# Performance work log

Hardware: AMD Instinct MI355X
Metric: run time of the kernel (lower is better)

## Reference

```python
import jax, jax.numpy as jnp
import numpy as np

B, T, D_MODEL = 4, 2048, 2048
H, KV, HD = 16, 8, 128  # num_heads, num_kv_heads, head_dim
EPS = 1e-6


def _rope_tables(T, hd, base=10000.0):
    inv_freq = 1.0 / (base ** (np.arange(0, hd, 2, dtype=np.float32) / hd))  # [hd/2]
    ang = np.arange(T, dtype=np.float32)[:, None] * inv_freq[None, :]        # [T, hd/2]
    cos = np.repeat(np.cos(ang), 2, axis=-1)                                 # [T, hd]
    sin = np.repeat(np.sin(ang), 2, axis=-1)
    return jnp.asarray(cos), jnp.asarray(sin)


def setup_inputs() -> dict:
    key = jax.random.key(0)
    ks = jax.random.split(key, 6)
    w_std = 0.02
    x = jax.random.normal(ks[0], (B, T, D_MODEL), dtype=jnp.float32)
    Wq = jax.random.normal(ks[1], (D_MODEL, H * HD), dtype=jnp.float32) * w_std
    Wk = jax.random.normal(ks[2], (D_MODEL, KV * HD), dtype=jnp.float32) * w_std
    Wv = jax.random.normal(ks[3], (D_MODEL, KV * HD), dtype=jnp.float32) * w_std
    Wo = jax.random.normal(ks[4], (H * HD, D_MODEL), dtype=jnp.float32) * w_std
    cos, sin = _rope_tables(T, HD)
    q_gamma = jnp.ones((HD,), dtype=jnp.float32)
    k_gamma = jnp.ones((HD,), dtype=jnp.float32)
    return {"x": x, "cos": cos, "sin": sin, "Wq": Wq, "Wk": Wk, "Wv": Wv,
            "Wo": Wo, "q_gamma": q_gamma, "k_gamma": k_gamma}


def _rmsnorm(h, gamma):
    # flax nn.RMSNorm over last axis, learnable scale
    var = jnp.mean(h * h, axis=-1, keepdims=True)
    return h * jax.lax.rsqrt(var + EPS) * gamma


def _rope(h, cos, sin):
    # h: [B, T, heads, HD]; interleaved rotation
    h_rot = jnp.stack([-h[..., 1::2], h[..., 0::2]], axis=-1)
    h_rot = h_rot.reshape(h.shape)
    return h * cos[None, :, None, :] + h_rot * sin[None, :, None, :]


def reference(x, cos, sin, Wq, Wk, Wv, Wo, q_gamma, k_gamma):
    Bx, Tx, _ = x.shape
    G = H // KV  # query groups per kv head
    q = (x @ Wq).reshape(Bx, Tx, H, HD)
    k = (x @ Wk).reshape(Bx, Tx, KV, HD)
    v = (x @ Wv).reshape(Bx, Tx, KV, HD)
    q = _rope(_rmsnorm(q, q_gamma), cos, sin)
    k = _rope(_rmsnorm(k, k_gamma), cos, sin)
    scale = 1.0 / jnp.sqrt(jnp.asarray(HD, dtype=x.dtype))
    qg = q.reshape(Bx, Tx, KV, G, HD)
    # scores: [B, KV, G, Tq, Tk]
    scores = jnp.einsum('btkgd,bskd->bkgts', qg, k) * scale
    p = jax.nn.softmax(scores, axis=-1)
    o = jnp.einsum('bkgts,bskd->btkgd', p, v).reshape(Bx, Tx, H * HD)
    return o @ Wo
```

## Files before the change

kernel.cpp:

```cpp
#include <hip/hip_runtime.h>


typedef unsigned short u16;
typedef unsigned int u32;
typedef __attribute__((ext_vector_type(8))) short bf16x8;
typedef __attribute__((ext_vector_type(4))) float f32x4;

__device__ __forceinline__ float bf2f(u16 v) {
    union { u32 u; float f; } x; x.u = ((u32)v) << 16; return x.f;
}
__device__ __forceinline__ u16 f2bf(float f) {
    union { float f; u32 u; } x; x.f = f;
    u32 u = x.u;
    return (u16)((u + 0x7FFFu + ((u >> 16) & 1u)) >> 16);
}
__device__ __forceinline__ u32 packtrunc(float a, float b) {
    union { float f; u32 u; } x, y; x.f = a; y.f = b;
    return (x.u >> 16) | (y.u & 0xffff0000u);
}
__device__ __forceinline__ f32x4 mfma_bf16(bf16x8 a, bf16x8 b, f32x4 c) {
    return __builtin_amdgcn_mfma_f32_16x16x32_bf16(a, b, c, 0, 0, 0);
}
__device__ __forceinline__ void gl_lds16(const u16* g, u16* l) {
    __builtin_amdgcn_global_load_lds((const __attribute__((address_space(1))) void*)g,
                                     (__attribute__((address_space(3))) void*)l, 16, 0, 0);
}

__global__ __launch_bounds__(256)
void transpose_f2b(const float* __restrict__ in, u16* __restrict__ out, int R, int C) {
    __shared__ float tile[32][33];
    const int tx = threadIdx.x & 31, ty = threadIdx.x >> 5;
    const long c0 = (long)blockIdx.x * 32, r0 = (long)blockIdx.y * 32;
#pragma unroll
    for (int i = 0; i < 4; i++)
        tile[ty + i * 8][tx] = in[(r0 + ty + i * 8) * C + c0 + tx];
    __syncthreads();
#pragma unroll
    for (int i = 0; i < 4; i++)
        out[(c0 + ty + i * 8) * R + r0 + tx] = f2bf(tile[tx][ty + i * 8]);
}

__global__ __launch_bounds__(256)
void cast_f2b(const float* __restrict__ in, u16* __restrict__ out) {
    const long i = ((long)blockIdx.x * 256 + threadIdx.x) * 8;
    float4 a = *(const float4*)(in + i);
    float4 b = *(const float4*)(in + i + 4);
    bf16x8 v;
    v[0] = (short)f2bf(a.x); v[1] = (short)f2bf(a.y);
    v[2] = (short)f2bf(a.z); v[3] = (short)f2bf(a.w);
    v[4] = (short)f2bf(b.x); v[5] = (short)f2bf(b.y);
    v[6] = (short)f2bf(b.z); v[7] = (short)f2bf(b.w);
    *(bf16x8*)(out + i) = v;
}

__global__ __launch_bounds__(256)
void transpose_v(const u16* __restrict__ qkv, u16* __restrict__ Vt) {
    __shared__ u16 tile[32][33];
    const int tx = threadIdx.x & 31, ty = threadIdx.x >> 5;
    const int d0 = blockIdx.x * 32;
    const int tok0 = blockIdx.y * 32;
#pragma unroll
    for (int i = 0; i < 4; i++)
        tile[ty + i * 8][tx] = qkv[(long)(tok0 + ty + i * 8) * 4096 + 3072 + d0 + tx];
    __syncthreads();
    const int b = tok0 >> 11;
    const long orow = (long)b * 1024 + d0;
    const int t0 = tok0 & 2047;
#pragma unroll
    for (int i = 0; i < 4; i++)
        Vt[(orow + ty + i * 8) * 2048 + t0 + tx] = tile[tx][ty + i * 8];
}

template <bool F32OUT>
__global__ __launch_bounds__(512, 2)
void gemm_bt_256(const u16* __restrict__ A, const u16* __restrict__ Bt,
                 void* __restrict__ Cp, int M, int N, int K) {
    __shared__ __align__(16) u16 As[2][256 * 64];
    __shared__ __align__(16) u16 Bs[2][256 * 64];
    const int tid = threadIdx.x, wid = tid >> 6, lane = tid & 63;
    const int q4 = lane >> 4, n16 = lane & 15;
    const int wr = (wid >> 2) * 128;
    const int wc = (wid & 3) * 64;

    const int nbx = N >> 8;
    const int nwg = nbx * (M >> 8);
    int id = (int)blockIdx.x;
    id = (id & 7) * (nwg >> 3) + (id >> 3);
    const long rowT = (long)(id / nbx) * 256;
    const long colT = (long)(id % nbx) * 256;

    const int srow = tid >> 3;
    const int gchunk = (tid & 7) ^ (srow & 7);
    const u16* Ag[4]; const u16* Bg[4];
#pragma unroll
    for (int i = 0; i < 4; i++) {
        Ag[i] = A  + (rowT + i * 64 + srow) * K + gchunk * 8;
        Bg[i] = Bt + (colT + i * 64 + srow) * K + gchunk * 8;
    }
    const int ldst = wid * 512 + lane * 8;

    auto stage = [&](int buf, int kt) {
#pragma unroll
        for (int i = 0; i < 4; i++)
            gl_lds16(Ag[i] + kt, &As[buf][i * 4096 + ldst]);
#pragma unroll
        for (int i = 0; i < 4; i++)
            gl_lds16(Bg[i] + kt, &Bs[buf][i * 4096 + ldst]);
    };

    f32x4 acc[8][4];
#pragma unroll
    for (int i = 0; i < 8; i++)
#pragma unroll
        for (int j = 0; j < 4; j++) acc[i][j] = (f32x4){0.f, 0.f, 0.f, 0.f};

    const int fs = n16 & 7;

    stage(0, 0);
    asm volatile("s_waitcnt vmcnt(0)" ::: "memory");
    __builtin_amdgcn_s_barrier();

    const int NT = K >> 6;
    for (int t = 0; t < NT; ++t) {
        const int buf = t & 1;
        if (t + 1 < NT) stage(buf ^ 1, (t + 1) << 6);

        const u16* Ac = As[buf];
        const u16* Bc = Bs[buf];
#pragma unroll
        for (int kk = 0; kk < 2; kk++) {
            const int slot = ((kk * 4 + q4) ^ fs) * 8;
            bf16x8 af[8], bv[4];
#pragma unroll
            for (int mb = 0; mb < 8; mb++)
                af[mb] = *(const bf16x8*)&Ac[(wr + mb * 16 + n16) * 64 + slot];
#pragma unroll
            for (int nb = 0; nb < 4; nb++)
                bv[nb] = *(const bf16x8*)&Bc[(wc + nb * 16 + n16) * 64 + slot];
#pragma unroll
            for (int mb = 0; mb < 8; mb++)
#pragma unroll
                for (int nb = 0; nb < 4; nb++)
                    acc[mb][nb] = mfma_bf16(af[mb], bv[nb], acc[mb][nb]);
        }
        asm volatile("s_waitcnt vmcnt(0)" ::: "memory");
        __builtin_amdgcn_s_barrier();
    }

#pragma unroll
    for (int mb = 0; mb < 8; mb++)
#pragma unroll
        for (int nb = 0; nb < 4; nb++)
#pragma unroll
            for (int r = 0; r < 4; r++) {
                long row = rowT + wr + mb * 16 + q4 * 4 + r;
                long col = colT + wc + nb * 16 + n16;
                if (F32OUT) ((float*)Cp)[row * N + col] = acc[mb][nb][r];
                else        ((u16*)Cp)[row * N + col]   = f2bf(acc[mb][nb][r]);
            }
}

__global__ __launch_bounds__(256)
void rmsnorm_rope(u16* __restrict__ qkv, const float* __restrict__ cosT,
                  const float* __restrict__ sinT, const float* __restrict__ qg,
                  const float* __restrict__ kg) {
    const int w = blockIdx.x * 4 + (threadIdx.x >> 6);
    const int lane = threadIdx.x & 63;
    const int token = w / 24;
    const int hv = w - token * 24;
    const long base = (long)token * 4096 + (hv < 16 ? hv * 128 : 2048 + (hv - 16) * 128);
    const float* g = (hv < 16) ? qg : kg;
    const int t = token & 2047;

    u32 pair = *(const u32*)(qkv + base + 2 * lane);
    float a0 = bf2f((u16)(pair & 0xffffu));
    float a1 = bf2f((u16)(pair >> 16));
    float ss = a0 * a0 + a1 * a1;
#pragma unroll
    for (int off = 32; off > 0; off >>= 1) ss += __shfl_xor(ss, off);
    float rs = rsqrtf(ss * (1.0f / 128.0f) + 1e-6f);
    float h0 = a0 * rs * g[2 * lane];
    float h1 = a1 * rs * g[2 * lane + 1];
    float2 cp = *(const float2*)(cosT + (long)t * 128 + 2 * lane);
    float2 sp = *(const float2*)(sinT + (long)t * 128 + 2 * lane);
    float o0 = h0 * cp.x - h1 * sp.x;
    float o1 = h1 * cp.y + h0 * sp.y;
    if (hv < 16) {
        const float QS = 0.08838834764831845f * 1.4426950408889634f;
        o0 *= QS; o1 *= QS;
    }
    *(u32*)(qkv + base + 2 * lane) = ((u32)f2bf(o0)) | (((u32)f2bf(o1)) << 16);
}

__global__ __launch_bounds__(256)
void flash_attn(const u16* __restrict__ qkv, const u16* __restrict__ Vt,
                u16* __restrict__ attn) {
    __shared__ __align__(16) u16 Ks[2][64 * 128];
    __shared__ __align__(16) u16 Vs[2][128 * 64];
    const int tid = threadIdx.x, wid = tid >> 6, lane = tid & 63;
    const int q4 = lane >> 4, n16 = lane & 15;

    const int bid = (int)(blockIdx.x + (blockIdx.y << 4));
    const int xq  = (bid >> 3) & 15;
    const int hy  = ((bid >> 7) << 3) | (bid & 7);
    const int b = hy >> 4, h = hy & 15;
    const int kvh = h >> 1;
    const long rowbase = (long)b * 2048;
    const long qbase = rowbase + (long)xq * 128 + wid * 32;

    const u16* Kbase = qkv + rowbase * 4096 + 2048 + kvh * 128;
    const u16* Vbase = Vt + ((long)(b * 8 + kvh) * 128) * 2048;

    const int krow_off = lane >> 4;
    const int kslot = lane & 15;
    int ktr[4], kgc[4];
#pragma unroll
    for (int i = 0; i < 4; i++) {
        int rho = wid * 16 + i * 4 + krow_off;
        ktr[i] = (rho & 32) | ((rho & 12) << 1) | ((rho & 16) >> 2) | (rho & 3);
        kgc[i] = kslot ^ (rho & 7);
    }
    const int vrow_off = lane >> 3;
    const int vslot = lane & 7;
    const int vg = vslot ^ vrow_off;

    auto stage = [&](int buf, int kt) {
#pragma unroll
        for (int i = 0; i < 4; i++)
            gl_lds16(Kbase + (long)(kt + ktr[i]) * 4096 + kgc[i] * 8,
                     &Ks[buf][(wid * 16 + i * 4) * 128 + lane * 8]);
#pragma unroll
        for (int i = 0; i < 4; i++) {
            int d = wid * 32 + i * 8 + vrow_off;
            gl_lds16(Vbase + (long)d * 2048 + kt + vg * 8,
                     &Vs[buf][(wid * 32 + i * 8) * 64 + lane * 8]);
        }
    };

    bf16x8 qf[2][4];
#pragma unroll
    for (int qb = 0; qb < 2; qb++) {
        const u16* p = qkv + (qbase + qb * 16 + n16) * 4096 + h * 128;
#pragma unroll
        for (int c = 0; c < 4; c++) qf[qb][c] = *(const bf16x8*)(p + c * 32 + q4 * 8);
    }

    f32x4 o[2][8];
#pragma unroll
    for (int i = 0; i < 2; i++)
#pragma unroll
        for (int j = 0; j < 8; j++) o[i][j] = (f32x4){0.f, 0.f, 0.f, 0.f};
    f32x4 l_acc[2] = {(f32x4){0.f, 0.f, 0.f, 0.f}, (f32x4){0.f, 0.f, 0.f, 0.f}};

    bf16x8 ones;
#pragma unroll
    for (int j = 0; j < 8; j++) ones[j] = (short)0x3f80;

    const int swz = n16 & 7;

    stage(0, 0);
    asm volatile("s_waitcnt vmcnt(0)" ::: "memory");
    __builtin_amdgcn_s_barrier();

    int cur = 0;
    for (int kt = 0; kt < 2048; kt += 64) {
        if (kt + 64 < 2048) stage(cur ^ 1, kt + 64);

        const u16* KsC = Ks[cur];
        const u16* VsC = Vs[cur];

        f32x4 s[2][4];
#pragma unroll
        for (int qb = 0; qb < 2; qb++)
#pragma unroll
            for (int kb = 0; kb < 4; kb++) s[qb][kb] = (f32x4){0.f, 0.f, 0.f, 0.f};
#pragma unroll
        for (int c = 0; c < 4; c++) {
            bf16x8 kf[4];
#pragma unroll
            for (int kb = 0; kb < 4; kb++) {
                int slot = (c * 4 + q4) ^ swz;
                kf[kb] = *(const bf16x8*)&KsC[(kb * 16 + n16) * 128 + slot * 8];
            }
            __builtin_amdgcn_s_setprio(1);
#pragma unroll
            for (int qb = 0; qb < 2; qb++)
#pragma unroll
                for (int kb = 0; kb < 4; kb++)
                    s[qb][kb] = mfma_bf16(kf[kb], qf[qb][c], s[qb][kb]);
            __builtin_amdgcn_s_setprio(0);
        }

        u32 pw[2][8];
#pragma unroll
        for (int qb = 0; qb < 2; qb++)
#pragma unroll
            for (int kb = 0; kb < 4; kb++) {
                float p0 = exp2f(s[qb][kb][0]);
                float p1 = exp2f(s[qb][kb][1]);
                float p2 = exp2f(s[qb][kb][2]);
                float p3 = exp2f(s[qb][kb][3]);
                pw[qb][kb * 2]     = packtrunc(p0, p1);
                pw[qb][kb * 2 + 1] = packtrunc(p2, p3);
            }

#pragma unroll
        for (int kc = 0; kc < 2; kc++) {
            bf16x8 vf[8];
#pragma unroll
            for (int nbh = 0; nbh < 8; nbh++) {
                int slot = (kc * 4 + q4) ^ swz;
                vf[nbh] = *(const bf16x8*)&VsC[(nbh * 16 + n16) * 64 + slot * 8];
            }
            __builtin_amdgcn_s_setprio(1);
#pragma unroll
            for (int qb = 0; qb < 2; qb++) {
                union { u32 w[4]; bf16x8 v; } pu;
                pu.w[0] = pw[qb][kc * 4];
                pu.w[1] = pw[qb][kc * 4 + 1];
                pu.w[2] = pw[qb][kc * 4 + 2];
                pu.w[3] = pw[qb][kc * 4 + 3];
                l_acc[qb] = mfma_bf16(pu.v, ones, l_acc[qb]);
#pragma unroll
                for (int nbh = 0; nbh < 8; nbh++)
                    o[qb][nbh] = mfma_bf16(pu.v, vf[nbh], o[qb][nbh]);
            }
            __builtin_amdgcn_s_setprio(0);
        }

        asm volatile("s_waitcnt vmcnt(0)" ::: "memory");
        __builtin_amdgcn_s_barrier();
        cur ^= 1;
    }

#pragma unroll
    for (int qb = 0; qb < 2; qb++) {
        float linv[4];
#pragma unroll
        for (int r = 0; r < 4; r++) linv[r] = 1.0f / l_acc[qb][r];
#pragma unroll
        for (int r = 0; r < 4; r++) {
            u16* op = attn + (qbase + qb * 16 + q4 * 4 + r) * 2048 + h * 128 + n16;
#pragma unroll
            for (int nbh = 0; nbh < 8; nbh++)
                op[nbh * 16] = f2bf(o[qb][nbh][r] * linv[r]);
        }
    }
}

extern "C" void kernel_launch(void* const* d_in, const int* in_sizes, int n_in,
                              void* d_out, int out_size, void* d_ws, size_t ws_size,
                              hipStream_t stream) {
    const float* x    = (const float*)d_in[0];
    const float* cosT = (const float*)d_in[1];
    const float* sinT = (const float*)d_in[2];
    const float* Wq   = (const float*)d_in[3];
    const float* Wk   = (const float*)d_in[4];
    const float* Wv   = (const float*)d_in[5];
    const float* Wo   = (const float*)d_in[6];
    const float* qg   = (const float*)d_in[7];
    const float* kg   = (const float*)d_in[8];
    float* out = (float*)d_out;

    char* ws = (char*)d_ws;
    u16* Bt_qkv = (u16*)(ws);
    u16* Vt     = (u16*)(ws);
    u16* Bt_o   = (u16*)(ws + 16777216);
    u16* xb     = (u16*)(ws + 25165824);
    u16* attn   = (u16*)(ws + 25165824);
    u16* qkv    = (u16*)(ws + 58720256);

    transpose_f2b<<<dim3(64, 64), 256, 0, stream>>>(Wq, Bt_qkv, 2048, 2048);
    transpose_f2b<<<dim3(32, 64), 256, 0, stream>>>(Wk, Bt_qkv + (size_t)2048 * 2048, 2048, 1024);
    transpose_f2b<<<dim3(32, 64), 256, 0, stream>>>(Wv, Bt_qkv + (size_t)3072 * 2048, 2048, 1024);
    transpose_f2b<<<dim3(64, 64), 256, 0, stream>>>(Wo, Bt_o, 2048, 2048);
    cast_f2b<<<dim3(8192), 256, 0, stream>>>(x, xb);

    gemm_bt_256<false><<<dim3(512), 512, 0, stream>>>(xb, Bt_qkv, qkv, 8192, 4096, 2048);

    transpose_v<<<dim3(32, 256), 256, 0, stream>>>(qkv, Vt);
    rmsnorm_rope<<<dim3(49152), 256, 0, stream>>>(qkv, cosT, sinT, qg, kg);

    flash_attn<<<dim3(16, 64), 256, 0, stream>>>(qkv, Vt, attn);

    gemm_bt_256<true><<<dim3(256), 512, 0, stream>>>(attn, Bt_o, out, 8192, 2048, 2048);
}
```

Before: 558.7 us.

## Split GEMM LDS tiles into halves and interleave staged loads with MFMA phases

Splits the 256x64 A/B shared tiles into two 128-row halves per buffer. The main loop becomes four phases that issue the next tile's half-loads early, use partial vmcnt waits, and run MFMAs under raised wave priority, with barriers between phases. The aim is to overlap global-to-LDS traffic with matrix math and shorten register live ranges for the A fragments. It adds more barriers per K step, which could cost synchronization overhead and relies on precise waitcnt accounting for correctness.

```diff
diff --git a/kernel.cpp b/kernel.cpp
--- a/kernel.cpp
+++ b/kernel.cpp
@@ -75,12 +75,15 @@
 __global__ __launch_bounds__(512, 2)
 void gemm_bt_256(const u16* __restrict__ A, const u16* __restrict__ Bt,
                  void* __restrict__ Cp, int M, int N, int K) {
-    __shared__ __align__(16) u16 As[2][256 * 64];
-    __shared__ __align__(16) u16 Bs[2][256 * 64];
+    __shared__ __align__(16) u16 As[2][2][128 * 64];
+    __shared__ __align__(16) u16 Bs[2][2][128 * 64];
     const int tid = threadIdx.x, wid = tid >> 6, lane = tid & 63;
     const int q4 = lane >> 4, n16 = lane & 15;
     const int wr = (wid >> 2) * 128;
     const int wc = (wid & 3) * 64;
+    const int Ah = wr >> 7;
+    const int Bh = wc >> 7;
+    const int brow0 = wc & 64;
 
     const int nbx = N >> 8;
     const int nwg = nbx * (M >> 8);
@@ -91,22 +94,26 @@
 
     const int srow = tid >> 3;
     const int gchunk = (tid & 7) ^ (srow & 7);
-    const u16* Ag[4]; const u16* Bg[4];
-#pragma unroll
-    for (int i = 0; i < 4; i++) {
-        Ag[i] = A  + (rowT + i * 64 + srow) * K + gchunk * 8;
-        Bg[i] = Bt + (colT + i * 64 + srow) * K + gchunk * 8;
-    }
+    const u16* Ag[2][2]; const u16* Bg[2][2];
+#pragma unroll
+    for (int h = 0; h < 2; h++)
+#pragma unroll
+        for (int l = 0; l < 2; l++) {
+            Ag[h][l] = A  + (rowT + h * 128 + l * 64 + srow) * K + gchunk * 8;
+            Bg[h][l] = Bt + (colT + h * 128 + l * 64 + srow) * K + gchunk * 8;
+        }
     const int ldst = wid * 512 + lane * 8;
 
-    auto stage = [&](int buf, int kt) {
-#pragma unroll
-        for (int i = 0; i < 4; i++)
-            gl_lds16(Ag[i] + kt, &As[buf][i * 4096 + ldst]);
-#pragma unroll
-        for (int i = 0; i < 4; i++)
-            gl_lds16(Bg[i] + kt, &Bs[buf][i * 4096 + ldst]);
+    auto stageA = [&](int par, int h, int kt) {
+#pragma unroll
+        for (int l = 0; l < 2; l++)
+            gl_lds16(Ag[h][l] + kt, &As[par][h][l * 4096 + ldst]);
     };
+    auto stageB = [&](int par, int h, int kt) {
+#pragma unroll
+        for (int l = 0; l < 2; l++)
+            gl_lds16(Bg[h][l] + kt, &Bs[par][h][l * 4096 + ldst]);
+    };
 
     f32x4 acc[8][4];
 #pragma unroll
@@ -116,35 +123,52 @@
 
     const int fs = n16 & 7;
 
-    stage(0, 0);
-    asm volatile("s_waitcnt vmcnt(0)" ::: "memory");
-    __builtin_amdgcn_s_barrier();
+    stageA(0, 0, 0); stageB(0, 0, 0); stageA(0, 1, 0); stageB(0, 1, 0);
 
     const int NT = K >> 6;
     for (int t = 0; t < NT; ++t) {
-        const int buf = t & 1;
-        if (t + 1 < NT) stage(buf ^ 1, (t + 1) << 6);
-
-        const u16* Ac = As[buf];
-        const u16* Bc = Bs[buf];
-#pragma unroll
-        for (int kk = 0; kk < 2; kk++) {
+        const int par = t & 1, nxt = par ^ 1;
+        const int ktn = (t + 1) << 6;
+        const bool more = (t + 1 < NT);
+        const u16* Acur = As[par][Ah];
+        const u16* Bcur = Bs[par][Bh];
+        bf16x8 bv[4];
+#pragma unroll
+        for (int ph = 0; ph < 4; ph++) {
+            const int kk = ph >> 1, mh = ph & 1;
+            if (ph == 0) {
+                if (more) {
+                    stageA(nxt, 0, ktn); stageB(nxt, 0, ktn);
+                    asm volatile("s_waitcnt vmcnt(4)" ::: "memory");
+                } else {
+                    asm volatile("s_waitcnt vmcnt(0)" ::: "memory");
+                }
+                __builtin_amdgcn_sched_barrier(0);
+                __builtin_amdgcn_s_barrier();
+            }
+            bf16x8 af[4];
             const int slot = ((kk * 4 + q4) ^ fs) * 8;
-            bf16x8 af[8], bv[4];
-#pragma unroll
-            for (int mb = 0; mb < 8; mb++)
-                af[mb] = *(const bf16x8*)&Ac[(wr + mb * 16 + n16) * 64 + slot];
-#pragma unroll
-            for (int nb = 0; nb < 4; nb++)
-                bv[nb] = *(const bf16x8*)&Bc[(wc + nb * 16 + n16) * 64 + slot];
-#pragma unroll
-            for (int mb = 0; mb < 8; mb++)
+#pragma unroll
+            for (int mb = 0; mb < 4; mb++)
+                af[mb] = *(const bf16x8*)&Acur[((mh * 4 + mb) * 16 + n16) * 64 + slot];
+            if (mh == 0) {
 #pragma unroll
                 for (int nb = 0; nb < 4; nb++)
-                    acc[mb][nb] = mfma_bf16(af[mb], bv[nb], acc[mb][nb]);
-        }
-        asm volatile("s_waitcnt vmcnt(0)" ::: "memory");
-        __builtin_amdgcn_s_barrier();
+                    bv[nb] = *(const bf16x8*)&Bcur[(brow0 + nb * 16 + n16) * 64 + slot];
+            }
+            if (ph == 1 && more) { stageA(nxt, 1, ktn); stageB(nxt, 1, ktn); }
+            if (ph != 0) __builtin_amdgcn_s_barrier();
+            asm volatile("s_waitcnt lgkmcnt(0)" ::: "memory");
+            __builtin_amdgcn_sched_barrier(0);
+            __builtin_amdgcn_s_setprio(1);
+#pragma unroll
+            for (int mb = 0; mb < 4; mb++)
+#pragma unroll
+                for (int nb = 0; nb < 4; nb++)
+                    acc[mh * 4 + mb][nb] = mfma_bf16(af[mb], bv[nb], acc[mh * 4 + mb][nb]);
+            __builtin_amdgcn_s_setprio(0);
+            __builtin_amdgcn_s_barrier();
+        }
     }
 
 #pragma unroll
```

New measurement: 575.4 us. +3.0%, slower.
